# Performance work log

Hardware: AMD Instinct MI355X
Metric: run time of the kernel (lower is better)

The kernel has to match this reference:

```python
import jax, jax.numpy as jnp
import numpy as np

V, H, L, NH, MAXS = 32000, 1024, 6, 16, 2048
HD = H // NH
FF = 4 * H
EPS = 1e-5


def _ln(x, s, b):
    m = jnp.mean(x, axis=-1, keepdims=True)
    v = jnp.mean(jnp.square(x - m), axis=-1, keepdims=True)
    return (x - m) * jax.lax.rsqrt(v + EPS) * s + b


def setup_inputs() -> dict:
    key = jax.random.key(0)
    ks = jax.random.split(key, 12)
    s = 0.02
    inp = {
        "input_ids": jax.random.randint(ks[0], (2, 1024), 0, V, dtype=jnp.int64),
        "token_emb": jax.random.normal(ks[1], (V, H), jnp.float32) * s,
        "pos_emb": jax.random.normal(ks[2], (MAXS, H), jnp.float32) * s,
        "ln1_s": jnp.ones((L, H), jnp.float32),
        "ln1_b": jnp.zeros((L, H), jnp.float32),
        "qkv_w": jax.random.normal(ks[3], (L, H, 3 * H), jnp.float32) * s,
        "qkv_b": jnp.zeros((L, 3 * H), jnp.float32),
        "out_w": jax.random.normal(ks[4], (L, H, H), jnp.float32) * s,
        "out_b": jnp.zeros((L, H), jnp.float32),
        "ln2_s": jnp.ones((L, H), jnp.float32),
        "ln2_b": jnp.zeros((L, H), jnp.float32),
        "w1": jax.random.normal(ks[5], (L, H, FF), jnp.float32) * s,
        "b1": jnp.zeros((L, FF), jnp.float32),
        "w2": jax.random.normal(ks[6], (L, FF, H), jnp.float32) * s,
        "b2": jnp.zeros((L, H), jnp.float32),
        "lnf_s": jnp.ones((H,), jnp.float32),
        "lnf_b": jnp.zeros((H,), jnp.float32),
        "lm_w": jax.random.normal(ks[7], (H, V), jnp.float32) * s,
    }
    return inp


def reference(input_ids, token_emb, pos_emb, ln1_s, ln1_b, qkv_w, qkv_b,
              out_w, out_b, ln2_s, ln2_b, w1, b1, w2, b2, lnf_s, lnf_b, lm_w):
    B, S = input_ids.shape
    x = token_emb[input_ids] + pos_emb[:S][None]  # [B,S,H]; dropout = identity (eval)
    for i in range(L):
        # --- attention block ---
        h = _ln(x, ln1_s[i], ln1_b[i])
        qkv = h @ qkv_w[i] + qkv_b[i]                      # [B,S,3H]
        q, k, v = jnp.split(qkv, 3, axis=-1)
        q = q.reshape(B, S, NH, HD)
        k = k.reshape(B, S, NH, HD)
        v = v.reshape(B, S, NH, HD)
        scores = jnp.einsum('bqhd,bkhd->bhqk', q, k) / jnp.sqrt(jnp.float32(HD))
        attn = jax.nn.softmax(scores, axis=-1)             # non-causal, as in source
        o = jnp.einsum('bhqk,bkhd->bqhd', attn, v).reshape(B, S, H)
        x = x + o @ out_w[i] + out_b[i]
        # --- mlp block ---
        h = _ln(x, ln2_s[i], ln2_b[i])
        h = jax.nn.gelu(h @ w1[i] + b1[i], approximate=False)
        x = x + h @ w2[i] + b2[i]
    x = _ln(x, lnf_s, lnf_b)
    logits = x @ lm_w                                      # [B,S,V]
    return logits
```

## Files before the change

### kernel.cpp

```cpp
#include <hip/hip_runtime.h>
#include <hip/hip_bf16.h>
#include <cstdint>
#include <cstddef>

typedef __bf16 bf16;
typedef __attribute__((ext_vector_type(8))) __bf16 bf16x8;
typedef __attribute__((ext_vector_type(4))) __bf16 bf16x4;
typedef __attribute__((ext_vector_type(4))) float f32x4;

__device__ __forceinline__ f32x4 mfma16(bf16x8 a, bf16x8 b, f32x4 c) {
    return __builtin_amdgcn_mfma_f32_16x16x32_bf16(a, b, c, 0, 0, 0);
}

__device__ __forceinline__ void async_copy16(const void* g, void* l) {
    __builtin_amdgcn_global_load_lds((const __attribute__((address_space(1))) void*)g,
                                     (__attribute__((address_space(3))) void*)l,
                                     16, 0, 0);
}

template<int Ncnt> __device__ __forceinline__ void waitv();
template<> __device__ __forceinline__ void waitv<0>() { asm volatile("s_waitcnt vmcnt(0)" ::: "memory"); }
template<> __device__ __forceinline__ void waitv<2>() { asm volatile("s_waitcnt vmcnt(2)" ::: "memory"); }
template<> __device__ __forceinline__ void waitv<3>() { asm volatile("s_waitcnt vmcnt(3)" ::: "memory"); }
template<> __device__ __forceinline__ void waitv<4>() { asm volatile("s_waitcnt vmcnt(4)" ::: "memory"); }

__device__ __forceinline__ void wait_g(int n) {
    if (n == 2) waitv<2>();
    else if (n == 3) waitv<3>();
    else waitv<4>();
}

__device__ __forceinline__ void ln_vec(f32x4 v, const float* __restrict__ sc,
                                       const float* __restrict__ bi, bf16* __restrict__ out,
                                       int row, int t, float* red)
{
    float s = v[0] + v[1] + v[2] + v[3];
    float q = v[0]*v[0] + v[1]*v[1] + v[2]*v[2] + v[3]*v[3];
    #pragma unroll
    for (int o = 1; o < 64; o <<= 1) { s += __shfl_xor(s, o); q += __shfl_xor(q, o); }
    const int wv = t >> 6, lane = t & 63;
    if (lane == 0) { red[wv] = s; red[4 + wv] = q; }
    __syncthreads();
    s = red[0] + red[1] + red[2] + red[3];
    q = red[4] + red[5] + red[6] + red[7];
    const float mean = s * (1.f / 1024.f);
    const float var  = q * (1.f / 1024.f) - mean * mean;
    const float rstd = rsqrtf(var + 1e-5f);
    const f32x4 scv = ((const f32x4*)sc)[t];
    const f32x4 biv = ((const f32x4*)bi)[t];
    bf16x4 o4;
    #pragma unroll
    for (int j = 0; j < 4; j++) o4[j] = (bf16)((v[j] - mean) * rstd * scv[j] + biv[j]);
    *(bf16x4*)(out + (size_t)row * 1024 + t * 4) = o4;
}

__device__ __forceinline__ void ln_body(const float* __restrict__ x, const float* __restrict__ sc,
                                        const float* __restrict__ bi, bf16* __restrict__ out,
                                        int row, int t, float* red)
{
    const f32x4 v = ((const f32x4*)(x + (size_t)row * 1024))[t];
    ln_vec(v, sc, bi, out, row, t, red);
}

__device__ __forceinline__ void wcvt_body(const float* __restrict__ W, bf16* __restrict__ BT,
                                          int K, int N, int bid, int tidx, float (*tile)[65])
{
    const int nx = N >> 6;
    const int n0 = (bid % nx) << 6, k0 = (bid / nx) << 6;
    const int tx = tidx & 15, ty = tidx >> 4;
    #pragma unroll
    for (int r = 0; r < 4; r++) {
        const f32x4 v = *(const f32x4*)&W[(size_t)(k0 + ty + r*16) * N + n0 + tx*4];
        tile[ty + r*16][tx*4 + 0] = v[0];
        tile[ty + r*16][tx*4 + 1] = v[1];
        tile[ty + r*16][tx*4 + 2] = v[2];
        tile[ty + r*16][tx*4 + 3] = v[3];
    }
    __syncthreads();
    #pragma unroll
    for (int r = 0; r < 4; r++) {
        const int n = ty + r*16;
        bf16x4 o;
        #pragma unroll
        for (int j = 0; j < 4; j++) o[j] = (bf16)tile[tx*4 + j][n];
        *(bf16x4*)&BT[(size_t)(n0 + n) * K + k0 + tx*4] = o;
    }
}

__global__ __launch_bounds__(256)
void front_kernel(const int* __restrict__ ids, const float* __restrict__ te,
                  const float* __restrict__ pe, float* __restrict__ x,
                  const float* __restrict__ sc, const float* __restrict__ bi,
                  bf16* __restrict__ out,
                  const float* __restrict__ qkvw0, bf16* __restrict__ wTq,
                  const float* __restrict__ lmw, bf16* __restrict__ wTlm,
                  const float* __restrict__ outw, bf16* __restrict__ wTo_all)
{
    __shared__ float tile[64][65];
    __shared__ float red[8];
    const int bid = blockIdx.x, t = threadIdx.x;
    if (bid < 2048) {
        const int s = bid & 1023;
        const int id = ids[bid];
        const f32x4 a = ((const f32x4*)(te + (size_t)id * 1024))[t];
        const f32x4 b = ((const f32x4*)(pe + (size_t)s * 1024))[t];
        const f32x4 v = a + b;
        ((f32x4*)(x + (size_t)bid * 1024))[t] = v;
        ln_vec(v, sc, bi, out, bid, t, red);
    } else if (bid < 2048 + 768) {
        wcvt_body(qkvw0, wTq, 1024, 3072, bid - 2048, t, tile);
    } else if (bid < 2048 + 768 + 8000) {
        wcvt_body(lmw, wTlm, 1024, 32000, bid - 2816, t, tile);
    } else {
        const int wb = bid - 10816;
        const int l = wb >> 8;
        wcvt_body(outw + (size_t)l * 1024 * 1024, wTo_all + (size_t)l * 1024 * 1024,
                  1024, 1024, wb & 255, t, tile);
    }
}

__global__ __launch_bounds__(256)
void fused_ln_wcvt(const float* __restrict__ x, const float* __restrict__ sc,
                   const float* __restrict__ bi, bf16* __restrict__ out,
                   const float* __restrict__ W1, bf16* __restrict__ BT1, int K1, int N1, int nb1,
                   const float* __restrict__ W2, bf16* __restrict__ BT2, int K2, int N2)
{
    __shared__ float tile[64][65];
    __shared__ float red[8];
    const int bid = blockIdx.x, t = threadIdx.x;
    if (bid < 2048) {
        ln_body(x, sc, bi, out, bid, t, red);
    } else {
        const int wb = bid - 2048;
        if (wb < nb1) wcvt_body(W1, BT1, K1, N1, wb, t, tile);
        else          wcvt_body(W2, BT2, K2, N2, wb - nb1, t, tile);
    }
}

__global__ __launch_bounds__(256)
void attn_kernel(const bf16* __restrict__ qkv, const bf16* __restrict__ vT,
                 bf16* __restrict__ attno)
{
    __shared__ __align__(16) bf16 Ksh[128 * 64];
    __shared__ __align__(16) bf16 Vt[64 * 128];
    __shared__ __align__(16) bf16 Plds[4][16][132];

    const int bid = blockIdx.x, tid = threadIdx.x;
    const int b = (bid & 31) >> 4, h = bid & 15;
    const int qb = bid >> 5;
    const int lane = tid & 63, wave = tid >> 6;
    const bf16* base = qkv + (size_t)b * 1024 * 3072;
    const bf16* vbase = vT + (size_t)(b*16 + h) * 64 * 1024;
    const int qrow0 = qb * 64 + wave * 16;
    const int l15 = lane & 15;

    bf16x8 aQ[2];
    {
        const int qr = qrow0 + l15;
        const bf16* qp = base + (size_t)qr * 3072 + h * 64 + ((lane >> 4) << 3);
        aQ[0] = *(const bf16x8*)qp;
        aQ[1] = *(const bf16x8*)(qp + 32);
    }
    float m_i[4] = {-1e30f, -1e30f, -1e30f, -1e30f};
    float l_i[4] = {0.f, 0.f, 0.f, 0.f};
    f32x4 acc[4];
    #pragma unroll
    for (int nb = 0; nb < 4; nb++) acc[nb] = f32x4{0.f, 0.f, 0.f, 0.f};

    const int swzA = (((lane >> 4)     ^ (lane & 7)) << 3);
    const int swzB = (((4 + (lane >> 4)) ^ (lane & 7)) << 3);

    for (int ck = 0; ck < 8; ck++) {
        __syncthreads();
        #pragma unroll
        for (int p = 0; p < 4; p++) {
            const int c = p * 256 + tid;
            const int rw = c >> 3;
            const int kc = (c & 7) ^ (rw & 7);
            async_copy16(base + (size_t)(ck*128 + rw) * 3072 + 1024 + h*64 + kc*8, &Ksh[c * 8]);
        }
        #pragma unroll
        for (int p = 0; p < 4; p++) {
            const int c = p * 256 + tid;
            const int rw = c >> 4;
            const int kc = (c & 15) ^ (rw & 7);
            async_copy16(vbase + (size_t)rw * 1024 + ck*128 + kc*8, &Vt[c * 8]);
        }
        waitv<4>();
        __builtin_amdgcn_sched_barrier(0);
        __builtin_amdgcn_s_barrier();

        f32x4 sc[8];
        #pragma unroll
        for (int kk = 0; kk < 4; kk++) {
            const int kr0 = (kk*32 + l15) * 64;
            const int kr1 = kr0 + 16*64;
            f32x4 z{0.f, 0.f, 0.f, 0.f};
            z = mfma16(aQ[0], *(const bf16x8*)&Ksh[kr0 + swzA], z);
            z = mfma16(aQ[1], *(const bf16x8*)&Ksh[kr0 + swzB], z);
            sc[2*kk] = z;
            f32x4 z2{0.f, 0.f, 0.f, 0.f};
            z2 = mfma16(aQ[0], *(const bf16x8*)&Ksh[kr1 + swzA], z2);
            z2 = mfma16(aQ[1], *(const bf16x8*)&Ksh[kr1 + swzB], z2);
            sc[2*kk+1] = z2;
        }

        float c[4];
        #pragma unroll
        for (int i = 0; i < 4; i++) {
            float t = sc[0][i];
            #pragma unroll
            for (int e = 1; e < 8; e++) t = fmaxf(t, sc[e][i]);
            #pragma unroll
            for (int o = 1; o < 16; o <<= 1) t = fmaxf(t, __shfl_xor(t, o));
            t *= 0.125f;
            const float mnew = fmaxf(m_i[i], t);
            c[i] = __expf(m_i[i] - mnew);
            float p[8];
            float rs = 0.f;
            #pragma unroll
            for (int e = 0; e < 8; e++) {
                p[e] = __expf(fmaf(sc[e][i], 0.125f, -mnew));
                rs += p[e];
            }
            #pragma unroll
            for (int o = 1; o < 16; o <<= 1) rs += __shfl_xor(rs, o);
            l_i[i] = l_i[i] * c[i] + rs;
            m_i[i] = mnew;
            const int pr = ((lane >> 4) << 2) + i;
            #pragma unroll
            for (int e = 0; e < 8; e++)
                Plds[wave][pr][(e >> 1) * 32 + (e & 1) * 16 + l15] = (bf16)p[e];
        }

        waitv<0>();
        __builtin_amdgcn_sched_barrier(0);
        __builtin_amdgcn_s_barrier();

        #pragma unroll
        for (int nb = 0; nb < 4; nb++) {
            f32x4 a = acc[nb];
            a[0] *= c[0]; a[1] *= c[1]; a[2] *= c[2]; a[3] *= c[3];
            acc[nb] = a;
        }
        #pragma unroll
        for (int kk = 0; kk < 4; kk++) {
            const bf16x8 aP = *(const bf16x8*)&Plds[wave][l15][kk*32 + ((lane >> 4) << 3)];
            #pragma unroll
            for (int nb = 0; nb < 4; nb++) {
                const int r = nb*16 + l15;
                const int chk = (kk*4 + (lane >> 4)) ^ (r & 7);
                const bf16x8 bV = *(const bf16x8*)&Vt[r*128 + chk*8];
                acc[nb] = mfma16(aP, bV, acc[nb]);
            }
        }
    }
    #pragma unroll
    for (int nb = 0; nb < 4; nb++) {
        #pragma unroll
        for (int i = 0; i < 4; i++) {
            const int row = qrow0 + ((lane >> 4) << 2) + i;
            const float o = acc[nb][i] / l_i[i];
            attno[(size_t)(b*1024 + row) * 1024 + h*64 + nb*16 + l15] = (bf16)o;
        }
    }
}

template<int BM, int BN, int EPI, int KSPLIT>
__global__ __launch_bounds__(512, 2)
void gemm256_kernel(const bf16* __restrict__ A, const bf16* __restrict__ BT,
                    const float* __restrict__ bias, float* __restrict__ resid,
                    bf16* __restrict__ outb, float* __restrict__ outf,
                    bf16* __restrict__ vt, int N, int K)
{
    constexpr int MT = 2048 / BM;
    constexpr int FM = BM / 32;
    constexpr int FN = BN / 64;
    constexpr int HM = FM / 2;
    constexpr int ACH = BM * 4;
    constexpr int BCH = BN * 4;
    constexpr int LA = (ACH + 511) >> 9;
    constexpr int LB = (BCH + 511) >> 9;
    constexpr int ASUB = BM * 32;
    constexpr int BSUB = BN * 32;
    extern __shared__ __align__(16) char smem_raw[];
    bf16* smem = (bf16*)smem_raw;

    const int nwg = gridDim.x;
    const int q = nwg >> 3, rr = nwg & 7;
    const int xcd = blockIdx.x & 7, ix = blockIdx.x >> 3;
    const int nid = (xcd < rr ? xcd * (q + 1) : rr * (q + 1) + (xcd - rr) * q) + ix;
    const int tiles = nwg / KSPLIT;
    const int ks = nid / tiles;
    const int tile = nid % tiles;
    const int bm = tile % MT, bn = tile / MT;

    const int tid = threadIdx.x, lane = tid & 63, wave = tid >> 6;
    const int wr = wave >> 2, wc = wave & 3;

    const int myB = ((BCH & 511) == 0) ? (BCH >> 9)
                    : ((tid < (BCH & 511)) ? (BCH >> 9) + 1 : (BCH >> 9));
    const int wcount = LA + myB;

    f32x4 acc[FM][FN];
    #pragma unroll
    for (int m = 0; m < FM; m++)
        #pragma unroll
        for (int n = 0; n < FN; n++) acc[m][n] = f32x4{0.f, 0.f, 0.f, 0.f};

    const bf16* Abase = A  + (size_t)bm * BM * K;
    const bf16* Bbase = BT + (size_t)bn * BN * K;
    const int Ts = (K >> 6) / KSPLIT;
    const int t0 = ks * Ts;

    const int l15 = lane & 15;
    const int swz = (((lane >> 4) ^ ((l15 >> 1) & 3)) << 3);
    const int arow0 = wr * (BM / 2) + l15;
    const int brow0 = wc * (BN / 4) + l15;

#define ABASE_(p_, ks_) (((p_)*2 + (ks_)) * ASUB)
#define BBASE_(p_, ks_) (4*ASUB + ((p_)*2 + (ks_)) * BSUB)
#define STAGE_A(p_, kt_, ks_) { _Pragma("unroll") for (int i = 0; i < LA; i++) { \
    const int c = tid + i * 512; \
    if ((ACH & 511) == 0 || c < ACH) { \
      const int rw = c >> 2; \
      const int kc = (c & 3) ^ ((rw >> 1) & 3); \
      async_copy16(Abase + (size_t)rw * K + (kt_)*64 + (ks_)*32 + kc*8, \
                   &smem[ABASE_(p_, ks_) + c*8]); } } }
#define STAGE_B(p_, kt_, ks_) { _Pragma("unroll") for (int i = 0; i < LB; i++) { \
    const int c = tid + i * 512; \
    if ((BCH & 511) == 0 || c < BCH) { \
      const int rw = c >> 2; \
      const int kc = (c & 3) ^ ((rw >> 1) & 3); \
      async_copy16(Bbase + (size_t)rw * K + (kt_)*64 + (ks_)*32 + kc*8, \
                   &smem[BBASE_(p_, ks_) + c*8]); } } }
#define LOAD_B(p_, ks_) { _Pragma("unroll") for (int n = 0; n < FN; n++) \
    bfv[n] = *(const bf16x8*)&smem[BBASE_(p_, ks_) + (brow0 + n*16)*32 + swz]; }
#define LOAD_A(p_, ks_, mg) { _Pragma("unroll") for (int m = 0; m < HM; m++) \
    af[m] = *(const bf16x8*)&smem[ABASE_(p_, ks_) + (arow0 + ((mg)*HM + m)*16)*32 + swz]; }
#define QUAD(mg) { __builtin_amdgcn_s_setprio(1); \
    _Pragma("unroll") for (int m = 0; m < HM; m++) \
      _Pragma("unroll") for (int n = 0; n < FN; n++) \
        acc[(mg)*HM + m][n] = mfma16(af[m], bfv[n], acc[(mg)*HM + m][n]); \
    __builtin_amdgcn_s_setprio(0); }

    STAGE_A(0, t0, 0); STAGE_B(0, t0, 0); STAGE_A(0, t0, 1); STAGE_B(0, t0, 1);
    wait_g(wcount);
    __builtin_amdgcn_s_barrier();

    for (int tl = 0; tl < Ts; tl++) {
        const int b = tl & 1;
        const int kt1 = t0 + tl + 1;
        const bool more = (tl + 1) < Ts;
        bf16x8 af[HM], bfv[FN];
        LOAD_B(b, 0); LOAD_A(b, 0, 0);
        if (more) STAGE_A(b ^ 1, kt1, 0);
        __builtin_amdgcn_s_barrier();
        QUAD(0);
        __builtin_amdgcn_s_barrier();
        LOAD_A(b, 0, 1);
        if (more) STAGE_B(b ^ 1, kt1, 0);
        __builtin_amdgcn_s_barrier();
        QUAD(1);
        if (more) wait_g(wcount); else waitv<0>();
        __builtin_amdgcn_s_barrier();
        LOAD_B(b, 1); LOAD_A(b, 1, 0);
        if (more) STAGE_A(b ^ 1, kt1, 1);
        __builtin_amdgcn_s_barrier();
        QUAD(0);
        __builtin_amdgcn_s_barrier();
        LOAD_A(b, 1, 1);
        if (more) STAGE_B(b ^ 1, kt1, 1);
        __builtin_amdgcn_s_barrier();
        QUAD(1);
        if (more) wait_g(wcount);
        __builtin_amdgcn_s_barrier();
    }

    const int er = bm * BM + wr * (BM / 2) + ((lane >> 4) << 2);
    const int ec = bn * BN + wc * (BN / 4) + l15;
    #pragma unroll
    for (int n = 0; n < FN; n++) {
        const int col = ec + n * 16;
        const float bv = (EPI == 3) ? 0.f : ((KSPLIT > 1 && ks != 0) ? 0.f : bias[col]);
        #pragma unroll
        for (int m = 0; m < FM; m++) {
            const int row0 = er + m * 16;
            if constexpr (EPI == 4) {
                if (col < 2048) {
                    #pragma unroll
                    for (int i = 0; i < 4; i++)
                        outb[(size_t)(row0 + i) * N + col] = (bf16)(acc[m][n][i] + bv);
                } else {
                    bf16x4 o4;
                    #pragma unroll
                    for (int i = 0; i < 4; i++) o4[i] = (bf16)(acc[m][n][i] + bv);
                    const int b_ = row0 >> 10, tok = row0 & 1023;
                    *(bf16x4*)&vt[((size_t)(b_ * 1024 + (col - 2048))) * 1024 + tok] = o4;
                }
            } else {
                #pragma unroll
                for (int i = 0; i < 4; i++) {
                    const float v = acc[m][n][i] + bv;
                    const size_t off = (size_t)(row0 + i) * N + col;
                    if constexpr (EPI == 0) outb[off] = (bf16)v;
                    else if constexpr (EPI == 1) {
                        if constexpr (KSPLIT > 1) atomicAdd(&resid[off], v);
                        else resid[off] += v;
                    }
                    else if constexpr (EPI == 2) {
                        outb[off] = (bf16)(0.5f * v * (1.f + erff(v * 0.70710678118f)));
                    } else {
                        outf[off] = v;
                    }
                }
            }
        }
    }
#undef ABASE_
#undef BBASE_
#undef STAGE_A
#undef STAGE_B
#undef LOAD_A
#undef LOAD_B
#undef QUAD
}

extern "C" void kernel_launch(void* const* d_in, const int* in_sizes, int n_in,
                              void* d_out, int out_size, void* d_ws, size_t ws_size,
                              hipStream_t stream)
{
    const int*   ids     = (const int*)  d_in[0];
    const float* tok_emb = (const float*)d_in[1];
    const float* pos_emb = (const float*)d_in[2];
    const float* ln1_s   = (const float*)d_in[3];
    const float* ln1_b   = (const float*)d_in[4];
    const float* qkv_w   = (const float*)d_in[5];
    const float* qkv_b   = (const float*)d_in[6];
    const float* out_w   = (const float*)d_in[7];
    const float* out_b   = (const float*)d_in[8];
    const float* ln2_s   = (const float*)d_in[9];
    const float* ln2_b   = (const float*)d_in[10];
    const float* w1      = (const float*)d_in[11];
    const float* b1      = (const float*)d_in[12];
    const float* w2      = (const float*)d_in[13];
    const float* b2      = (const float*)d_in[14];
    const float* lnf_s   = (const float*)d_in[15];
    const float* lnf_b   = (const float*)d_in[16];
    const float* lm_w    = (const float*)d_in[17];

    char* ws = (char*)d_ws;
    float* x    = (float*)ws;  ws += (size_t)2048 * 1024 * 4;
    bf16*  h    = (bf16*)ws;   ws += (size_t)2048 * 1024 * 2;
    bf16*  qkvb = (bf16*)ws;   ws += (size_t)2048 * 3072 * 2;
    bf16*  attno= (bf16*)ws;   ws += (size_t)2048 * 1024 * 2;
    bf16*  vT   = (bf16*)ws;   ws += (size_t)32 * 64 * 1024 * 2;
    bf16*  ff   = (bf16*)ws;   ws += (size_t)2048 * 4096 * 2;
    bf16*  wTq  = (bf16*)ws;   ws += (size_t)3072 * 1024 * 2;
    bf16*  wTo_all = (bf16*)ws; ws += (size_t)6 * 1024 * 1024 * 2;
    bf16*  wT1  = (bf16*)ws;   ws += (size_t)4096 * 1024 * 2;
    bf16*  wT2  = (bf16*)ws;   ws += (size_t)1024 * 4096 * 2;
    bf16*  wTlm = (bf16*)ws;   ws += (size_t)32000 * 1024 * 2;

    for (int l = 0; l < 6; l++) {
        if (l == 0) {
            front_kernel<<<12352, 256, 0, stream>>>(
                ids, tok_emb, pos_emb, x, ln1_s, ln1_b, h,
                qkv_w, wTq, lm_w, wTlm, out_w, wTo_all);
        } else {
            fused_ln_wcvt<<<2048 + 768, 256, 0, stream>>>(
                x, ln1_s + l*1024, ln1_b + l*1024, h,
                qkv_w + (size_t)l*1024*3072, wTq, 1024, 3072, 768,
                nullptr, nullptr, 0, 0);
        }
        gemm256_kernel<128,192,4,1><<<256, 512, 81920, stream>>>(
            h, wTq, qkv_b + l*3072, nullptr, qkvb, nullptr, vT, 3072, 1024);
        attn_kernel<<<512, 256, 0, stream>>>(qkvb, vT, attno);
        gemm256_kernel<128,256,1,4><<<256, 512, 98304, stream>>>(
            attno, wTo_all + (size_t)l*1024*1024, out_b + l*1024, x, nullptr, nullptr, nullptr, 1024, 1024);
        fused_ln_wcvt<<<2048 + 1024 + 1024, 256, 0, stream>>>(
            x, ln2_s + l*1024, ln2_b + l*1024, h,
            w1 + (size_t)l*1024*4096, wT1, 1024, 4096, 1024,
            w2 + (size_t)l*4096*1024, wT2, 4096, 1024);
        gemm256_kernel<128,256,2,1><<<256, 512, 98304, stream>>>(
            h, wT1, b1 + l*4096, nullptr, ff, nullptr, nullptr, 4096, 1024);
        gemm256_kernel<128,256,1,4><<<256, 512, 98304, stream>>>(
            ff, wT2, b2 + l*1024, x, nullptr, nullptr, nullptr, 1024, 4096);
    }
    fused_ln_wcvt<<<2048, 256, 0, stream>>>(
        x, lnf_s, lnf_b, h,
        nullptr, nullptr, 0, 0, 0,
        nullptr, nullptr, 0, 0);
    gemm256_kernel<256,256,3,1><<<8*125, 512, 131072, stream>>>(
        h, wTlm, nullptr, nullptr, nullptr, (float*)d_out, nullptr, 32000, 1024);
}
```

Measured before the change: 1.289 ms.

## Overlap weight transposes with attention kernel and double-buffer QKV weights

Moves the fp32-to-bf16 weight conversion for the next layer's QKV weights and the current layer's MLP weights into the attention launch as extra blocks, so they run alongside the attention work instead of inside the LayerNorm kernels. LayerNorm becomes a standalone kernel. The converted QKV weight buffer is double-buffered so the next layer's weights can be written while the current ones are still in use. The attention blocks now share one LDS buffer sized for both roles, and the conversion blocks compete with attention blocks for compute units.

```diff
diff --git a/kernel.cpp b/kernel.cpp
--- a/kernel.cpp
+++ b/kernel.cpp
@@ -120,32 +120,41 @@
 }
 
 __global__ __launch_bounds__(256)
-void fused_ln_wcvt(const float* __restrict__ x, const float* __restrict__ sc,
-                   const float* __restrict__ bi, bf16* __restrict__ out,
-                   const float* __restrict__ W1, bf16* __restrict__ BT1, int K1, int N1, int nb1,
-                   const float* __restrict__ W2, bf16* __restrict__ BT2, int K2, int N2)
-{
-    __shared__ float tile[64][65];
+void ln_kernel(const float* __restrict__ x, const float* __restrict__ sc,
+               const float* __restrict__ bi, bf16* __restrict__ out)
+{
     __shared__ float red[8];
-    const int bid = blockIdx.x, t = threadIdx.x;
-    if (bid < 2048) {
-        ln_body(x, sc, bi, out, bid, t, red);
-    } else {
-        const int wb = bid - 2048;
-        if (wb < nb1) wcvt_body(W1, BT1, K1, N1, wb, t, tile);
-        else          wcvt_body(W2, BT2, K2, N2, wb - nb1, t, tile);
-    }
+    ln_body(x, sc, bi, out, blockIdx.x, threadIdx.x, red);
 }
 
 __global__ __launch_bounds__(256)
-void attn_kernel(const bf16* __restrict__ qkv, const bf16* __restrict__ vT,
-                 bf16* __restrict__ attno)
-{
-    __shared__ __align__(16) bf16 Ksh[128 * 64];
-    __shared__ __align__(16) bf16 Vt[64 * 128];
-    __shared__ __align__(16) bf16 Plds[4][16][132];
-
+void attn_wcvt_kernel(const bf16* __restrict__ qkv, const bf16* __restrict__ vT,
+                      bf16* __restrict__ attno,
+                      const float* __restrict__ qkvw_n, bf16* __restrict__ wTq_n,
+                      const float* __restrict__ w1, bf16* __restrict__ wT1,
+                      const float* __restrict__ w2, bf16* __restrict__ wT2)
+{
+    __shared__ __align__(16) char smem[49664];
     const int bid = blockIdx.x, tid = threadIdx.x;
+
+    if (bid >= 512) {
+        float (*tile)[65] = (float(*)[65])smem;
+        const int wb = bid - 512;
+        if (wb < 768) {
+            if (qkvw_n) wcvt_body(qkvw_n, wTq_n, 1024, 3072, wb, tid, tile);
+        } else if (wb < 768 + 1024) {
+            wcvt_body(w1, wT1, 1024, 4096, wb - 768, tid, tile);
+        } else {
+            wcvt_body(w2, wT2, 4096, 1024, wb - 1792, tid, tile);
+        }
+        return;
+    }
+
+    bf16* Ksh = (bf16*)smem;
+    bf16* Vt  = (bf16*)(smem + 16384);
+    bf16* Plds = (bf16*)(smem + 32768);
+#define PLDS(w_, r_, c_) Plds[(((w_) << 4) + (r_)) * 132 + (c_)]
+
     const int b = (bid & 31) >> 4, h = bid & 15;
     const int qb = bid >> 5;
     const int lane = tid & 63, wave = tid >> 6;
@@ -230,7 +239,7 @@
             const int pr = ((lane >> 4) << 2) + i;
             #pragma unroll
             for (int e = 0; e < 8; e++)
-                Plds[wave][pr][(e >> 1) * 32 + (e & 1) * 16 + l15] = (bf16)p[e];
+                PLDS(wave, pr, (e >> 1) * 32 + (e & 1) * 16 + l15) = (bf16)p[e];
         }
 
         waitv<0>();
@@ -245,7 +254,7 @@
         }
         #pragma unroll
         for (int kk = 0; kk < 4; kk++) {
-            const bf16x8 aP = *(const bf16x8*)&Plds[wave][l15][kk*32 + ((lane >> 4) << 3)];
+            const bf16x8 aP = *(const bf16x8*)&PLDS(wave, l15, kk*32 + ((lane >> 4) << 3));
             #pragma unroll
             for (int nb = 0; nb < 4; nb++) {
                 const int r = nb*16 + l15;
@@ -264,6 +273,7 @@
             attno[(size_t)(b*1024 + row) * 1024 + h*64 + nb*16 + l15] = (bf16)o;
         }
     }
+#undef PLDS
 }
 
 template<int BM, int BN, int EPI, int KSPLIT>
@@ -456,41 +466,38 @@
     bf16*  attno= (bf16*)ws;   ws += (size_t)2048 * 1024 * 2;
     bf16*  vT   = (bf16*)ws;   ws += (size_t)32 * 64 * 1024 * 2;
     bf16*  ff   = (bf16*)ws;   ws += (size_t)2048 * 4096 * 2;
-    bf16*  wTq  = (bf16*)ws;   ws += (size_t)3072 * 1024 * 2;
+    bf16*  wTq2 = (bf16*)ws;   ws += (size_t)2 * 3072 * 1024 * 2;
     bf16*  wTo_all = (bf16*)ws; ws += (size_t)6 * 1024 * 1024 * 2;
     bf16*  wT1  = (bf16*)ws;   ws += (size_t)4096 * 1024 * 2;
     bf16*  wT2  = (bf16*)ws;   ws += (size_t)1024 * 4096 * 2;
     bf16*  wTlm = (bf16*)ws;   ws += (size_t)32000 * 1024 * 2;
 
     for (int l = 0; l < 6; l++) {
+        bf16* wTq_cur = wTq2 + (size_t)(l & 1) * 3072 * 1024;
+        bf16* wTq_nxt = wTq2 + (size_t)((l + 1) & 1) * 3072 * 1024;
         if (l == 0) {
             front_kernel<<<12352, 256, 0, stream>>>(
                 ids, tok_emb, pos_emb, x, ln1_s, ln1_b, h,
-                qkv_w, wTq, lm_w, wTlm, out_w, wTo_all);
+                qkv_w, wTq_cur, lm_w, wTlm, out_w, wTo_all);
         } else {
-            fused_ln_wcvt<<<2048 + 768, 256, 0, stream>>>(
-                x, ln1_s + l*1024, ln1_b + l*1024, h,
-                qkv_w + (size_t)l*1024*3072, wTq, 1024, 3072, 768,
-                nullptr, nullptr, 0, 0);
+            ln_kernel<<<2048, 256, 0, stream>>>(x, ln1_s + l*1024, ln1_b + l*1024, h);
         }
         gemm256_kernel<128,192,4,1><<<256, 512, 81920, stream>>>(
-            h, wTq, qkv_b + l*3072, nullptr, qkvb, nullptr, vT, 3072, 1024);
-        attn_kernel<<<512, 256, 0, stream>>>(qkvb, vT, attno);
+            h, wTq_cur, qkv_b + l*3072, nullptr, qkvb, nullptr, vT, 3072, 1024);
+        attn_wcvt_kernel<<<3328, 256, 0, stream>>>(
+            qkvb, vT, attno,
+            (l < 5) ? qkv_w + (size_t)(l+1)*1024*3072 : nullptr, wTq_nxt,
+            w1 + (size_t)l*1024*4096, wT1,
+            w2 + (size_t)l*4096*1024, wT2);
         gemm256_kernel<128,256,1,4><<<256, 512, 98304, stream>>>(
             attno, wTo_all + (size_t)l*1024*1024, out_b + l*1024, x, nullptr, nullptr, nullptr, 1024, 1024);
-        fused_ln_wcvt<<<2048 + 1024 + 1024, 256, 0, stream>>>(
-            x, ln2_s + l*1024, ln2_b + l*1024, h,
-            w1 + (size_t)l*1024*4096, wT1, 1024, 4096, 1024,
-            w2 + (size_t)l*4096*1024, wT2, 4096, 1024);
+        ln_kernel<<<2048, 256, 0, stream>>>(x, ln2_s + l*1024, ln2_b + l*1024, h);
         gemm256_kernel<128,256,2,1><<<256, 512, 98304, stream>>>(
             h, wT1, b1 + l*4096, nullptr, ff, nullptr, nullptr, 4096, 1024);
         gemm256_kernel<128,256,1,4><<<256, 512, 98304, stream>>>(
             ff, wT2, b2 + l*1024, x, nullptr, nullptr, nullptr, 1024, 4096);
     }
-    fused_ln_wcvt<<<2048, 256, 0, stream>>>(
-        x, lnf_s, lnf_b, h,
-        nullptr, nullptr, 0, 0, 0,
-        nullptr, nullptr, 0, 0);
+    ln_kernel<<<2048, 256, 0, stream>>>(x, lnf_s, lnf_b, h);
     gemm256_kernel<256,256,3,1><<<8*125, 512, 131072, stream>>>(
         h, wTlm, nullptr, nullptr, nullptr, (float*)d_out, nullptr, 32000, 1024);
 }
```

Result: no change. 1.270 ms (-1.4%).
